# Performance work log

Measured on AMD Instinct MI355X. Metric: run time of the kernel, lower is better.

## Reference

```python
import jax, jax.numpy as jnp
import numpy as np

B, T, D, H = 256, 512, 64, 128


def setup_inputs() -> dict:
    key = jax.random.key(0)
    ks = jax.random.split(key, 24)
    inp = {
        'values': jax.random.normal(ks[0], (B, T, D), jnp.float32),
        'masks': jax.random.randint(ks[1], (B, T, D), 0, 2).astype(jnp.float32),
        'deltas': jax.random.uniform(ks[2], (B, T, D), jnp.float32),
        'empirical_mean': jax.random.normal(ks[3], (D,), jnp.float32),
        'X_filledLOCF': jax.random.normal(ks[4], (B, T, D), jnp.float32),
        # parameters (xavier-ish scale for matrices, uniform for vectors)
        'w_gamma_x': jax.random.uniform(ks[5], (D,), jnp.float32),
        'w_gamma_h': jax.random.normal(ks[6], (D, H), jnp.float32) * (2.0 / (D + H)) ** 0.5,
        'w_rx': jax.random.normal(ks[7], (D, H), jnp.float32) * (2.0 / (D + H)) ** 0.5,
        'w_rh': jax.random.normal(ks[8], (H, H), jnp.float32) * (1.0 / H) ** 0.5,
        'w_rm': jax.random.normal(ks[9], (D, H), jnp.float32) * (2.0 / (D + H)) ** 0.5,
        'w_zx': jax.random.normal(ks[10], (D, H), jnp.float32) * (2.0 / (D + H)) ** 0.5,
        'w_zh': jax.random.normal(ks[11], (H, H), jnp.float32) * (1.0 / H) ** 0.5,
        'w_zm': jax.random.normal(ks[12], (D, H), jnp.float32) * (2.0 / (D + H)) ** 0.5,
        'w_hx': jax.random.normal(ks[13], (D, H), jnp.float32) * (2.0 / (D + H)) ** 0.5,
        'w_hh': jax.random.normal(ks[14], (H, H), jnp.float32) * (1.0 / H) ** 0.5,
        'w_hm': jax.random.normal(ks[15], (D, H), jnp.float32) * (2.0 / (D + H)) ** 0.5,
        'b_gamma_x': jax.random.uniform(ks[16], (D,), jnp.float32),
        'b_gamma_h': jax.random.uniform(ks[17], (H,), jnp.float32),
        'b_r': jax.random.uniform(ks[18], (H,), jnp.float32),
        'b_z': jax.random.uniform(ks[19], (H,), jnp.float32),
        'b_h': jax.random.uniform(ks[20], (H,), jnp.float32),
    }
    return inp


def reference(values, masks, deltas, empirical_mean, X_filledLOCF,
              w_gamma_x, w_gamma_h, w_rx, w_rh, w_rm, w_zx, w_zh, w_zm,
              w_hx, w_hh, w_hm, b_gamma_x, b_gamma_h, b_r, b_z, b_h):
    b, t, d = values.shape
    h0 = jnp.zeros((b, w_gamma_h.shape[1]), values.dtype)

    def step(h, xs):
        x, m, dlt, xl = xs  # each [B, D]
        gamma_x = jnp.exp(-jax.nn.relu(w_gamma_x * dlt + b_gamma_x))      # [B, D]
        gamma_h = jnp.exp(-jax.nn.relu(dlt @ w_gamma_h + b_gamma_h))      # [B, H]
        x = m * x + (1 - m) * (gamma_x * xl + (1 - gamma_x) * empirical_mean)
        h = gamma_h * h
        z = jax.nn.sigmoid(x @ w_zx + h @ w_zh + m @ w_zm + b_z)
        r = jax.nn.sigmoid(x @ w_rx + h @ w_rh + m @ w_rm + b_r)
        h_tilde = jnp.tanh(x @ w_hx + (r * h) @ w_hh + m @ w_hm + b_h)
        h = (1 - z) * h + z * h_tilde
        return h, h

    # scan over time axis: [T, B, D]
    xs = (jnp.swapaxes(values, 0, 1), jnp.swapaxes(masks, 0, 1),
          jnp.swapaxes(deltas, 0, 1), jnp.swapaxes(X_filledLOCF, 0, 1))
    h_last, hs = jax.lax.scan(step, h0, xs)
    hidden_tensor = jnp.swapaxes(hs, 0, 1)  # [B, T, H]
    return hidden_tensor, h_last
```

## Files before the change

### kernel.cpp

```cpp
#include <hip/hip_runtime.h>
#include <hip/hip_fp16.h>

#define B_ 256
#define T_ 512
#define D_ 64
#define H_ 128
#define BB 16

typedef float f32x4 __attribute__((ext_vector_type(4)));
typedef short s16x4 __attribute__((ext_vector_type(4)));
typedef short s16x8 __attribute__((ext_vector_type(8)));
typedef __fp16 fp16x2 __attribute__((ext_vector_type(2)));
typedef _Float16 h16x4 __attribute__((ext_vector_type(4)));
typedef _Float16 f16x8v __attribute__((ext_vector_type(8)));

__device__ unsigned short g_W16[7 * 8 * 2 * 512];
__device__ float g_bias[512];

__device__ inline float fsig(float x) {
  return __builtin_amdgcn_rcpf(1.f + __expf(-x));
}
__device__ inline float ftanh(float x) {
  return 1.f - 2.f * __builtin_amdgcn_rcpf(1.f + __expf(2.f * x));
}
__device__ __forceinline__ f32x4 MFH(s16x8 a, s16x8 b, f32x4 c) {
  return __builtin_amdgcn_mfma_f32_16x16x32_f16(
      __builtin_bit_cast(f16x8v, a), __builtin_bit_cast(f16x8v, b), c, 0, 0, 0);
}
__device__ __forceinline__ f32x4 MFH2(s16x8 wfrag, f16x8v xfrag, f32x4 c) {
  return __builtin_amdgcn_mfma_f32_16x16x32_f16(
      __builtin_bit_cast(f16x8v, wfrag), xfrag, c, 0, 0, 0);
}

#define BAR()                                              \
  do {                                                     \
    asm volatile("s_waitcnt lgkmcnt(0)" ::: "memory");     \
    __builtin_amdgcn_s_barrier();                          \
  } while (0)

__global__ __launch_bounds__(64) void wprep(
    const float* __restrict__ wgh, const float* __restrict__ wzx,
    const float* __restrict__ wzm, const float* __restrict__ wrx,
    const float* __restrict__ wrm, const float* __restrict__ whx,
    const float* __restrict__ whm, const float* __restrict__ bgh,
    const float* __restrict__ bz, const float* __restrict__ br,
    const float* __restrict__ bh) {
  const int g = blockIdx.x, l = threadIdx.x;
  if (g < 112) {
    const float* mats[7] = {wgh, wzx, wzm, wrx, wrm, whx, whm};
    const int mat = g >> 4, sub = g & 15, ct = sub >> 1, tau = sub & 1;
    const float* W = mats[mat];
    const int base = ((mat * 8 + ct) * 2 + tau) * 512 + l * 8;
#pragma unroll
    for (int j = 0; j < 8; ++j) {
      const int k = 8 * (l >> 4) + j + 32 * tau;
      const int col = ct * 16 + (l & 15);
      g_W16[base + j] =
          __builtin_bit_cast(unsigned short, __float2half(W[k * 128 + col]));
    }
  } else {
    const int c = (g - 112) * 64 + l;
    float v = (c < 128)   ? bgh[c]
              : (c < 256) ? bz[c - 128]
              : (c < 384) ? br[c - 256]
                          : bh[c - 384];
    g_bias[c] = v;
  }
}

__global__ __launch_bounds__(256) void grud_pre_mfma(
    const float* __restrict__ values, const float* __restrict__ masks,
    const float* __restrict__ deltas, const float* __restrict__ emean,
    const float* __restrict__ locf, const float* __restrict__ w_gamma_x,
    const float* __restrict__ b_gamma_x, __half* __restrict__ A) {
  __shared__ __align__(16) char plds[25344];
  float* c_wg = (float*)(plds + 24576);
  float* c_bg = (float*)(plds + 24832);
  float* c_mn = (float*)(plds + 25088);

  const int tid = threadIdx.x;
  const int rowbase = blockIdx.x * 64;

  if (tid < 64) c_wg[tid] = w_gamma_x[tid];
  else if (tid < 128) c_bg[tid - 64] = b_gamma_x[tid - 64];
  else if (tid < 192) c_mn[tid - 128] = emean[tid - 128];
  __syncthreads();

  {
    const int r = tid >> 2;
    const int sp = tid & 3;
    const int swz = (r & 7) << 4;
#pragma unroll
    for (int ss = 0; ss < 2; ++ss) {
      const int s = sp + 4 * ss;
      const int k0 = 8 * s;
      const size_t gb = (size_t)(rowbase + r) * 64 + k0;
      const float4* vp = (const float4*)(values + gb);
      const float4* mp = (const float4*)(masks + gb);
      const float4* dp = (const float4*)(deltas + gb);
      const float4* lp = (const float4*)(locf + gb);
      float4 v0 = vp[0], v1 = vp[1], m0 = mp[0], m1 = mp[1];
      float4 d0 = dp[0], d1 = dp[1], l0 = lp[0], l1 = lp[1];
      float vv[8] = {v0.x, v0.y, v0.z, v0.w, v1.x, v1.y, v1.z, v1.w};
      float mm[8] = {m0.x, m0.y, m0.z, m0.w, m1.x, m1.y, m1.z, m1.w};
      float dd[8] = {d0.x, d0.y, d0.z, d0.w, d1.x, d1.y, d1.z, d1.w};
      float ll[8] = {l0.x, l0.y, l0.z, l0.w, l1.x, l1.y, l1.z, l1.w};
      s16x8 xe_, mv_, dl_;
#pragma unroll
      for (int j = 0; j < 8; ++j) {
        const int d_ = k0 + j;
        float gx = __expf(-fmaxf(c_wg[d_] * dd[j] + c_bg[d_], 0.f));
        float xo = mm[j] * vv[j] +
                   (1.f - mm[j]) * (gx * ll[j] + (1.f - gx) * c_mn[d_]);
        xe_[j] = __builtin_bit_cast(short, __float2half(xo));
        mv_[j] = __builtin_bit_cast(short, __float2half(mm[j]));
        dl_[j] = __builtin_bit_cast(short, __float2half(dd[j]));
      }
      const int ta = r * 128 + ((s * 16) ^ swz);
      *(s16x8*)(plds + ta) = xe_;
      *(s16x8*)(plds + 8192 + ta) = mv_;
      *(s16x8*)(plds + 16384 + ta) = dl_;
    }
  }
  __syncthreads();

  const int l = tid & 63;
  const int rt = tid >> 6;
  f16x8v xe0, xe1, mm0, mm1, dl0, dl1;
  {
    const int r = rt * 16 + (l & 15);
    const int swz = (r & 7) << 4;
    const int s0 = ((l >> 4) * 16) ^ swz;
    const int s1 = (((l >> 4) + 4) * 16) ^ swz;
    xe0 = *(const f16x8v*)(plds + r * 128 + s0);
    xe1 = *(const f16x8v*)(plds + r * 128 + s1);
    mm0 = *(const f16x8v*)(plds + 8192 + r * 128 + s0);
    mm1 = *(const f16x8v*)(plds + 8192 + r * 128 + s1);
    dl0 = *(const f16x8v*)(plds + 16384 + r * 128 + s0);
    dl1 = *(const f16x8v*)(plds + 16384 + r * 128 + s1);
  }

  const s16x8* Wb = (const s16x8*)g_W16;
  const int cj = (l >> 4) * 4;
  const int row = rowbase + rt * 16 + (l & 15);
  unsigned short* Aout = (unsigned short*)A + (size_t)row * 512;
#pragma unroll 4
  for (int ct = 0; ct < 32; ++ct) {
    const int g = ct >> 3, ctl = ct & 7;
    f32x4 acc = {0.f, 0.f, 0.f, 0.f};
    if (g == 0) {
      s16x8 B0 = Wb[(ctl * 2 + 0) * 64 + l];
      s16x8 B1 = Wb[(ctl * 2 + 1) * 64 + l];
      acc = MFH2(B0, dl0, acc);
      acc = MFH2(B1, dl1, acc);
    } else {
      const int mx = 2 * g - 1, mmat = 2 * g;
      s16x8 Bx0 = Wb[((mx * 8 + ctl) * 2 + 0) * 64 + l];
      s16x8 Bx1 = Wb[((mx * 8 + ctl) * 2 + 1) * 64 + l];
      s16x8 Bm0 = Wb[((mmat * 8 + ctl) * 2 + 0) * 64 + l];
      s16x8 Bm1 = Wb[((mmat * 8 + ctl) * 2 + 1) * 64 + l];
      acc = MFH2(Bx0, xe0, acc);
      acc = MFH2(Bx1, xe1, acc);
      acc = MFH2(Bm0, mm0, acc);
      acc = MFH2(Bm1, mm1, acc);
    }
    const f32x4 bv = *(const f32x4*)(g_bias + ct * 16 + cj);
    h16x4 outv;
#pragma unroll
    for (int j = 0; j < 4; ++j) {
      float v = acc[j] + bv[j];
      if (ct < 8) v = __expf(-fmaxf(v, 0.f));
      outv[j] = (_Float16)v;
    }
    *(h16x4*)(Aout + g * 128 + ctl * 16 + cj) = outv;
  }
}

#define STEP(T0, CUR, NXT)                                                  \
  do {                                                                      \
    const int t_ = (T0);                                                    \
    f32x4 Dz0 = {(float)CUR[1][0], (float)CUR[1][1],                        \
                 (float)CUR[1][2], (float)CUR[1][3]};                       \
    f32x4 Dr0 = {(float)CUR[2][0], (float)CUR[2][1],                        \
                 (float)CUR[2][2], (float)CUR[2][3]};                       \
    f32x4 Dh0 = {(float)CUR[3][0], (float)CUR[3][1],                        \
                 (float)CUR[3][2], (float)CUR[3][3]};                       \
    {                                         \
      const int t4 = (t_ + 4 < T_) ? t_ + 4 : T_ - 1;                       \
      const size_t r = ((size_t)bg * T_ + t4) * 128 + ci;                   \
      CUR[0] = Arows[r];       CUR[1] = Arows[r + 32];                      \
      CUR[2] = Arows[r + 64];  CUR[3] = Arows[r + 96];                      \
    }                                                                       \
    f32x4 Dz1 = {0, 0, 0, 0}, Dr1 = {0, 0, 0, 0};                           \
    {                                                                       \
      s16x8 bh0 = *(const s16x8*)(h_bf + off_rd[0]);                        \
      s16x8 bh1 = *(const s16x8*)(h_bf + off_rd[1]);                        \
      s16x8 bh2 = *(const s16x8*)(h_bf + off_rd[2]);                        \
      s16x8 bh3 = *(const s16x8*)(h_bf + off_rd[3]);                        \
      Dz0 = MFH(wzf[0], bh0, Dz0); Dr0 = MFH(wrf[0], bh0, Dr0);             \
      Dz1 = MFH(wzf[2], bh2, Dz1); Dr1 = MFH(wrf[2], bh2, Dr1);             \
      Dz0 = MFH(wzf[1], bh1, Dz0); Dr0 = MFH(wrf[1], bh1, Dr0);             \
      Dz1 = MFH(wzf[3], bh3, Dz1); Dr1 = MFH(wrf[3], bh3, Dr1);             \
    }                                                                       \
    f32x4 zz;                                                               \
    {                                                                       \
      float r0_ = fsig(Dr0[0] + Dr1[0]) * hsc[0];                           \
      float r1_ = fsig(Dr0[1] + Dr1[1]) * hsc[1];                           \
      float r2_ = fsig(Dr0[2] + Dr1[2]) * hsc[2];                           \
      float r3_ = fsig(Dr0[3] + Dr1[3]) * hsc[3];                           \
      zz[0] = fsig(Dz0[0] + Dz1[0]); zz[1] = fsig(Dz0[1] + Dz1[1]);         \
      zz[2] = fsig(Dz0[2] + Dz1[2]); zz[3] = fsig(Dz0[3] + Dz1[3]);         \
      union { fp16x2 h2[2]; s16x4 v; } u;                                   \
      u.h2[0] = __builtin_amdgcn_cvt_pkrtz(r0_, r1_);                       \
      u.h2[1] = __builtin_amdgcn_cvt_pkrtz(r2_, r3_);                       \
      *(s16x4*)(rh_bf + off_wr) = u.v;                                      \
    }                                                                       \
    BAR();                                                                  \
    f32x4 Dh1 = {0, 0, 0, 0};                                               \
    {                                                                       \
      s16x8 p0 = *(const s16x8*)(rh_bf + off_rd[0]);                        \
      s16x8 p1 = *(const s16x8*)(rh_bf + off_rd[1]);                        \
      s16x8 p2 = *(const s16x8*)(rh_bf + off_rd[2]);                        \
      s16x8 p3 = *(const s16x8*)(rh_bf + off_rd[3]);                        \
      Dh0 = MFH(whf[0], p0, Dh0); Dh1 = MFH(whf[2], p2, Dh1);               \
      Dh0 = MFH(whf[1], p1, Dh0); Dh1 = MFH(whf[3], p3, Dh1);               \
    }                                                                       \
    f32x4 hnv, hgv;                                                         \
    _Pragma("unroll")                                                       \
    for (int j = 0; j < 4; ++j) {                                           \
      float ht = ftanh(Dh0[j] + Dh1[j]);                                    \
      float hn = hsc[j] + zz[j] * (ht - hsc[j]);                            \
      hnv[j] = hn;                                                          \
      float hg = hn * (float)NXT[0][j];              \
      hgv[j] = hg;                                                          \
      hsc[j] = hg;                                                          \
    }                                                                       \
    {                                                                       \
      union { fp16x2 h2[2]; s16x4 v; } u;                                   \
      u.h2[0] = __builtin_amdgcn_cvt_pkrtz(hgv[0], hgv[1]);                 \
      u.h2[1] = __builtin_amdgcn_cvt_pkrtz(hgv[2], hgv[3]);                 \
      *(s16x4*)(h_bf + off_wr) = u.v;                                       \
    }                                                                       \
    *(f32x4*)(hid + ((size_t)bg * T_ + t_) * H_ + cb) = hnv;                \
    if (t_ == T_ - 1) *(f32x4*)(hlast + (size_t)bg * H_ + cb) = hnv;        \
    BAR();                                                                  \
  } while (0)

__global__ __launch_bounds__(512, 1) void grud_rec_mfma(
    const __half* __restrict__ A, const float* __restrict__ w_zh,
    const float* __restrict__ w_rh, const float* __restrict__ w_hh,
    float* __restrict__ hid, float* __restrict__ hlast) {
  const int tid = threadIdx.x;
  const int w = tid >> 6;
  const int lane = tid & 63;
  const int b = lane & 15;
  const int q = lane >> 4;
  const int cb = w * 16 + q * 4;
  const int bg = blockIdx.x * BB + b;

  __shared__ __align__(16) char lds[8192];
  char* h_bf = lds;
  char* rh_bf = lds + 4096;

  s16x8 wzf[4], wrf[4], whf[4];
#pragma unroll
  for (int tau = 0; tau < 4; ++tau) {
    s16x8 az, ar, ah;
#pragma unroll
    for (int j = 0; j < 8; ++j) {
      const int k = q * 8 + j + 32 * tau;
      az[j] = __builtin_bit_cast(short, (_Float16)w_zh[k * H_ + w * 16 + b]);
      ar[j] = __builtin_bit_cast(short, (_Float16)w_rh[k * H_ + w * 16 + b]);
      ah[j] = __builtin_bit_cast(short, (_Float16)w_hh[k * H_ + w * 16 + b]);
    }
    wzf[tau] = az; wrf[tau] = ar; whf[tau] = ah;
  }

  for (int i = tid; i < 8192 / 16; i += 512)
    ((f32x4*)lds)[i] = f32x4{0.f, 0.f, 0.f, 0.f};

  int off_rd[4];
#pragma unroll
  for (int tau = 0; tau < 4; ++tau) off_rd[tau] = tau * 1024 + lane * 16;
  const int off_wr =
      (w >> 1) * 1024 + (b + 16 * ((2 * w + (q >> 1)) & 3)) * 16 + 8 * (q & 1);

  const h16x4* Arows = (const h16x4*)A;
  const int ci = cb >> 2;

  h16x4 b0[4], b1[4], b2[4], b3[4];
  {
    const size_t r0 = ((size_t)bg * T_ + 0) * 128 + ci;
    b0[0] = Arows[r0]; b0[1] = Arows[r0 + 32];
    b0[2] = Arows[r0 + 64]; b0[3] = Arows[r0 + 96];
    const size_t r1 = ((size_t)bg * T_ + 1) * 128 + ci;
    b1[0] = Arows[r1]; b1[1] = Arows[r1 + 32];
    b1[2] = Arows[r1 + 64]; b1[3] = Arows[r1 + 96];
    const size_t r2 = ((size_t)bg * T_ + 2) * 128 + ci;
    b2[0] = Arows[r2]; b2[1] = Arows[r2 + 32];
    b2[2] = Arows[r2 + 64]; b2[3] = Arows[r2 + 96];
    const size_t r3 = ((size_t)bg * T_ + 3) * 128 + ci;
    b3[0] = Arows[r3]; b3[1] = Arows[r3 + 32];
    b3[2] = Arows[r3 + 64]; b3[3] = Arows[r3 + 96];
  }
  f32x4 hsc = {0.f, 0.f, 0.f, 0.f};
  __syncthreads();

  for (int tp = 0; tp < T_; tp += 4) {
    STEP(tp + 0, b0, b1);
    STEP(tp + 1, b1, b2);
    STEP(tp + 2, b2, b3);
    STEP(tp + 3, b3, b0);
  }
}

extern "C" void kernel_launch(void* const* d_in, const int* in_sizes, int n_in,
                              void* d_out, int out_size, void* d_ws, size_t ws_size,
                              hipStream_t stream) {
  const float* values = (const float*)d_in[0];
  const float* masks = (const float*)d_in[1];
  const float* deltas = (const float*)d_in[2];
  const float* emean = (const float*)d_in[3];
  const float* locf = (const float*)d_in[4];
  const float* w_gamma_x = (const float*)d_in[5];
  const float* w_gamma_h = (const float*)d_in[6];
  const float* w_rx = (const float*)d_in[7];
  const float* w_rh = (const float*)d_in[8];
  const float* w_rm = (const float*)d_in[9];
  const float* w_zx = (const float*)d_in[10];
  const float* w_zh = (const float*)d_in[11];
  const float* w_zm = (const float*)d_in[12];
  const float* w_hx = (const float*)d_in[13];
  const float* w_hh = (const float*)d_in[14];
  const float* w_hm = (const float*)d_in[15];
  const float* b_gamma_x = (const float*)d_in[16];
  const float* b_gamma_h = (const float*)d_in[17];
  const float* b_r = (const float*)d_in[18];
  const float* b_z = (const float*)d_in[19];
  const float* b_h = (const float*)d_in[20];

  float* hid = (float*)d_out;
  float* hlast = hid + (size_t)B_ * T_ * H_;
  __half* A = (__half*)d_ws;

  wprep<<<dim3(120), dim3(64), 0, stream>>>(
      w_gamma_h, w_zx, w_zm, w_rx, w_rm, w_hx, w_hm, b_gamma_h, b_z, b_r, b_h);
  grud_pre_mfma<<<dim3(B_ * T_ / 64), dim3(256), 0, stream>>>(
      values, masks, deltas, emean, locf, w_gamma_x, b_gamma_x, A);
  grud_rec_mfma<<<dim3(B_ / BB), dim3(512), 0, stream>>>(A, w_zh, w_rh, w_hh,
                                                         hid, hlast);
}
```

Before: 631.0 us.

## Process two 16-row batch groups per block to interleave independent recurrences

Each block now handles 32 batch rows as two independent 16-row groups (A and B), so their MFMA chains and activations interleave inside one step. The aim is to hide MFMA and LDS latency on the serial recurrence critical path with independent work, and to spread the per-step barrier cost over twice as many rows. In exchange the grid is halved to 8 blocks, so fewer CUs are used, and register pressure rises with the doubled prefetch buffers. The dual-accumulator split per gate is replaced by a single longer accumulation chain per group.

```diff
diff --git a/kernel.cpp b/kernel.cpp
--- a/kernel.cpp
+++ b/kernel.cpp
@@ -5,7 +5,7 @@
 #define T_ 512
 #define D_ 64
 #define H_ 128
-#define BB 16
+#define BB 32
 
 typedef float f32x4 __attribute__((ext_vector_type(4)));
 typedef short s16x4 __attribute__((ext_vector_type(4)));
@@ -179,70 +179,105 @@
 #define STEP(T0, CUR, NXT)                                                  \
   do {                                                                      \
     const int t_ = (T0);                                                    \
-    f32x4 Dz0 = {(float)CUR[1][0], (float)CUR[1][1],                        \
+    f32x4 DzA = {(float)CUR[1][0], (float)CUR[1][1],                        \
                  (float)CUR[1][2], (float)CUR[1][3]};                       \
-    f32x4 Dr0 = {(float)CUR[2][0], (float)CUR[2][1],                        \
+    f32x4 DrA = {(float)CUR[2][0], (float)CUR[2][1],                        \
                  (float)CUR[2][2], (float)CUR[2][3]};                       \
-    f32x4 Dh0 = {(float)CUR[3][0], (float)CUR[3][1],                        \
+    f32x4 DhA = {(float)CUR[3][0], (float)CUR[3][1],                        \
                  (float)CUR[3][2], (float)CUR[3][3]};                       \
-    {                                         \
+    f32x4 DzB = {(float)CUR[5][0], (float)CUR[5][1],                        \
+                 (float)CUR[5][2], (float)CUR[5][3]};                       \
+    f32x4 DrB = {(float)CUR[6][0], (float)CUR[6][1],                        \
+                 (float)CUR[6][2], (float)CUR[6][3]};                       \
+    f32x4 DhB = {(float)CUR[7][0], (float)CUR[7][1],                        \
+                 (float)CUR[7][2], (float)CUR[7][3]};                       \
+    {                            \
       const int t4 = (t_ + 4 < T_) ? t_ + 4 : T_ - 1;                       \
-      const size_t r = ((size_t)bg * T_ + t4) * 128 + ci;                   \
-      CUR[0] = Arows[r];       CUR[1] = Arows[r + 32];                      \
-      CUR[2] = Arows[r + 64];  CUR[3] = Arows[r + 96];                      \
-    }                                                                       \
-    f32x4 Dz1 = {0, 0, 0, 0}, Dr1 = {0, 0, 0, 0};                           \
+      const size_t rA = ((size_t)bgA * T_ + t4) * 128 + ci;                 \
+      const size_t rB = ((size_t)bgB * T_ + t4) * 128 + ci;                 \
+      CUR[0] = Arows[rA];       CUR[1] = Arows[rA + 32];                    \
+      CUR[2] = Arows[rA + 64];  CUR[3] = Arows[rA + 96];                    \
+      CUR[4] = Arows[rB];       CUR[5] = Arows[rB + 32];                    \
+      CUR[6] = Arows[rB + 64];  CUR[7] = Arows[rB + 96];                    \
+    }                                                                       \
     {                                                                       \
-      s16x8 bh0 = *(const s16x8*)(h_bf + off_rd[0]);                        \
-      s16x8 bh1 = *(const s16x8*)(h_bf + off_rd[1]);                        \
-      s16x8 bh2 = *(const s16x8*)(h_bf + off_rd[2]);                        \
-      s16x8 bh3 = *(const s16x8*)(h_bf + off_rd[3]);                        \
-      Dz0 = MFH(wzf[0], bh0, Dz0); Dr0 = MFH(wrf[0], bh0, Dr0);             \
-      Dz1 = MFH(wzf[2], bh2, Dz1); Dr1 = MFH(wrf[2], bh2, Dr1);             \
-      Dz0 = MFH(wzf[1], bh1, Dz0); Dr0 = MFH(wrf[1], bh1, Dr0);             \
-      Dz1 = MFH(wzf[3], bh3, Dz1); Dr1 = MFH(wrf[3], bh3, Dr1);             \
-    }                                                                       \
-    f32x4 zz;                                                               \
+      s16x8 hA0 = *(const s16x8*)(lds + off_rd[0]);                         \
+      s16x8 hA1 = *(const s16x8*)(lds + off_rd[1]);                         \
+      s16x8 hA2 = *(const s16x8*)(lds + off_rd[2]);                         \
+      s16x8 hA3 = *(const s16x8*)(lds + off_rd[3]);                         \
+      s16x8 hB0 = *(const s16x8*)(lds + 8192 + off_rd[0]);                  \
+      s16x8 hB1 = *(const s16x8*)(lds + 8192 + off_rd[1]);                  \
+      s16x8 hB2 = *(const s16x8*)(lds + 8192 + off_rd[2]);                  \
+      s16x8 hB3 = *(const s16x8*)(lds + 8192 + off_rd[3]);                  \
+      DzA = MFH(wzf[0], hA0, DzA); DzB = MFH(wzf[0], hB0, DzB);             \
+      DrA = MFH(wrf[0], hA0, DrA); DrB = MFH(wrf[0], hB0, DrB);             \
+      DzA = MFH(wzf[1], hA1, DzA); DzB = MFH(wzf[1], hB1, DzB);             \
+      DrA = MFH(wrf[1], hA1, DrA); DrB = MFH(wrf[1], hB1, DrB);             \
+      DzA = MFH(wzf[2], hA2, DzA); DzB = MFH(wzf[2], hB2, DzB);             \
+      DrA = MFH(wrf[2], hA2, DrA); DrB = MFH(wrf[2], hB2, DrB);             \
+      DzA = MFH(wzf[3], hA3, DzA); DzB = MFH(wzf[3], hB3, DzB);             \
+      DrA = MFH(wrf[3], hA3, DrA); DrB = MFH(wrf[3], hB3, DrB);             \
+    }                                                                       \
+    f32x4 zzA, zzB;                                                         \
     {                                                                       \
-      float r0_ = fsig(Dr0[0] + Dr1[0]) * hsc[0];                           \
-      float r1_ = fsig(Dr0[1] + Dr1[1]) * hsc[1];                           \
-      float r2_ = fsig(Dr0[2] + Dr1[2]) * hsc[2];                           \
-      float r3_ = fsig(Dr0[3] + Dr1[3]) * hsc[3];                           \
-      zz[0] = fsig(Dz0[0] + Dz1[0]); zz[1] = fsig(Dz0[1] + Dz1[1]);         \
-      zz[2] = fsig(Dz0[2] + Dz1[2]); zz[3] = fsig(Dz0[3] + Dz1[3]);         \
-      union { fp16x2 h2[2]; s16x4 v; } u;                                   \
-      u.h2[0] = __builtin_amdgcn_cvt_pkrtz(r0_, r1_);                       \
-      u.h2[1] = __builtin_amdgcn_cvt_pkrtz(r2_, r3_);                       \
-      *(s16x4*)(rh_bf + off_wr) = u.v;                                      \
+      union { fp16x2 h2[2]; s16x4 v; } uA, uB;                              \
+      float a0 = fsig(DrA[0]) * hscA[0], a1 = fsig(DrA[1]) * hscA[1];       \
+      float a2 = fsig(DrA[2]) * hscA[2], a3 = fsig(DrA[3]) * hscA[3];       \
+      float b0_ = fsig(DrB[0]) * hscB[0], b1_ = fsig(DrB[1]) * hscB[1];     \
+      float b2_ = fsig(DrB[2]) * hscB[2], b3_ = fsig(DrB[3]) * hscB[3];     \
+      zzA[0] = fsig(DzA[0]); zzA[1] = fsig(DzA[1]);                         \
+      zzA[2] = fsig(DzA[2]); zzA[3] = fsig(DzA[3]);                         \
+      zzB[0] = fsig(DzB[0]); zzB[1] = fsig(DzB[1]);                         \
+      zzB[2] = fsig(DzB[2]); zzB[3] = fsig(DzB[3]);                         \
+      uA.h2[0] = __builtin_amdgcn_cvt_pkrtz(a0, a1);                        \
+      uA.h2[1] = __builtin_amdgcn_cvt_pkrtz(a2, a3);                        \
+      uB.h2[0] = __builtin_amdgcn_cvt_pkrtz(b0_, b1_);                      \
+      uB.h2[1] = __builtin_amdgcn_cvt_pkrtz(b2_, b3_);                      \
+      *(s16x4*)(lds + 4096 + off_wr) = uA.v;                                \
+      *(s16x4*)(lds + 12288 + off_wr) = uB.v;                               \
     }                                                                       \
     BAR();                                                                  \
-    f32x4 Dh1 = {0, 0, 0, 0};                                               \
     {                                                                       \
-      s16x8 p0 = *(const s16x8*)(rh_bf + off_rd[0]);                        \
-      s16x8 p1 = *(const s16x8*)(rh_bf + off_rd[1]);                        \
-      s16x8 p2 = *(const s16x8*)(rh_bf + off_rd[2]);                        \
-      s16x8 p3 = *(const s16x8*)(rh_bf + off_rd[3]);                        \
-      Dh0 = MFH(whf[0], p0, Dh0); Dh1 = MFH(whf[2], p2, Dh1);               \
-      Dh0 = MFH(whf[1], p1, Dh0); Dh1 = MFH(whf[3], p3, Dh1);               \
-    }                                                                       \
-    f32x4 hnv, hgv;                                                         \
-    _Pragma("unroll")                                                       \
-    for (int j = 0; j < 4; ++j) {                                           \
-      float ht = ftanh(Dh0[j] + Dh1[j]);                                    \
-      float hn = hsc[j] + zz[j] * (ht - hsc[j]);                            \
-      hnv[j] = hn;                                                          \
-      float hg = hn * (float)NXT[0][j];              \
-      hgv[j] = hg;                                                          \
-      hsc[j] = hg;                                                          \
+      s16x8 pA0 = *(const s16x8*)(lds + 4096 + off_rd[0]);                  \
+      s16x8 pA1 = *(const s16x8*)(lds + 4096 + off_rd[1]);                  \
+      s16x8 pA2 = *(const s16x8*)(lds + 4096 + off_rd[2]);                  \
+      s16x8 pA3 = *(const s16x8*)(lds + 4096 + off_rd[3]);                  \
+      s16x8 pB0 = *(const s16x8*)(lds + 12288 + off_rd[0]);                 \
+      s16x8 pB1 = *(const s16x8*)(lds + 12288 + off_rd[1]);                 \
+      s16x8 pB2 = *(const s16x8*)(lds + 12288 + off_rd[2]);                 \
+      s16x8 pB3 = *(const s16x8*)(lds + 12288 + off_rd[3]);                 \
+      DhA = MFH(whf[0], pA0, DhA); DhB = MFH(whf[0], pB0, DhB);             \
+      DhA = MFH(whf[1], pA1, DhA); DhB = MFH(whf[1], pB1, DhB);             \
+      DhA = MFH(whf[2], pA2, DhA); DhB = MFH(whf[2], pB2, DhB);             \
+      DhA = MFH(whf[3], pA3, DhA); DhB = MFH(whf[3], pB3, DhB);             \
     }                                                                       \
     {                                                                       \
-      union { fp16x2 h2[2]; s16x4 v; } u;                                   \
-      u.h2[0] = __builtin_amdgcn_cvt_pkrtz(hgv[0], hgv[1]);                 \
-      u.h2[1] = __builtin_amdgcn_cvt_pkrtz(hgv[2], hgv[3]);                 \
-      *(s16x4*)(h_bf + off_wr) = u.v;                                       \
-    }                                                                       \
-    *(f32x4*)(hid + ((size_t)bg * T_ + t_) * H_ + cb) = hnv;                \
-    if (t_ == T_ - 1) *(f32x4*)(hlast + (size_t)bg * H_ + cb) = hnv;        \
+      f32x4 hnA, hnB;                                                       \
+      union { fp16x2 h2[2]; s16x4 v; } uA, uB;                              \
+      _Pragma("unroll")                                                     \
+      for (int j = 0; j < 4; ++j) {                                         \
+        float htA = ftanh(DhA[j]);                                          \
+        float ha = hscA[j] + zzA[j] * (htA - hscA[j]);                      \
+        hnA[j] = ha;                                                        \
+        hscA[j] = ha * (float)NXT[0][j];                                    \
+        float htB = ftanh(DhB[j]);                                          \
+        float hb = hscB[j] + zzB[j] * (htB - hscB[j]);                      \
+        hnB[j] = hb;                                                        \
+        hscB[j] = hb * (float)NXT[4][j];                                    \
+      }                                                                     \
+      uA.h2[0] = __builtin_amdgcn_cvt_pkrtz(hscA[0], hscA[1]);              \
+      uA.h2[1] = __builtin_amdgcn_cvt_pkrtz(hscA[2], hscA[3]);              \
+      uB.h2[0] = __builtin_amdgcn_cvt_pkrtz(hscB[0], hscB[1]);              \
+      uB.h2[1] = __builtin_amdgcn_cvt_pkrtz(hscB[2], hscB[3]);              \
+      *(s16x4*)(lds + off_wr) = uA.v;                                       \
+      *(s16x4*)(lds + 8192 + off_wr) = uB.v;                                \
+      *(f32x4*)(hid + ((size_t)bgA * T_ + t_) * H_ + cb) = hnA;             \
+      *(f32x4*)(hid + ((size_t)bgB * T_ + t_) * H_ + cb) = hnB;             \
+      if (t_ == T_ - 1) {                                                   \
+        *(f32x4*)(hlast + (size_t)bgA * H_ + cb) = hnA;                     \
+        *(f32x4*)(hlast + (size_t)bgB * H_ + cb) = hnB;                     \
+      }                                                                     \
+    }                                                                       \
     BAR();                                                                  \
   } while (0)
 
@@ -256,11 +291,10 @@
   const int b = lane & 15;
   const int q = lane >> 4;
   const int cb = w * 16 + q * 4;
-  const int bg = blockIdx.x * BB + b;
-
-  __shared__ __align__(16) char lds[8192];
-  char* h_bf = lds;
-  char* rh_bf = lds + 4096;
+  const int bgA = blockIdx.x * BB + b;
+  const int bgB = bgA + 16;
+
+  __shared__ __align__(16) char lds[16384];
 
   s16x8 wzf[4], wrf[4], whf[4];
 #pragma unroll
@@ -276,7 +310,7 @@
     wzf[tau] = az; wrf[tau] = ar; whf[tau] = ah;
   }
 
-  for (int i = tid; i < 8192 / 16; i += 512)
+  for (int i = tid; i < 16384 / 16; i += 512)
     ((f32x4*)lds)[i] = f32x4{0.f, 0.f, 0.f, 0.f};
 
   int off_rd[4];
@@ -288,22 +322,18 @@
   const h16x4* Arows = (const h16x4*)A;
   const int ci = cb >> 2;
 
-  h16x4 b0[4], b1[4], b2[4], b3[4];
-  {
-    const size_t r0 = ((size_t)bg * T_ + 0) * 128 + ci;
-    b0[0] = Arows[r0]; b0[1] = Arows[r0 + 32];
-    b0[2] = Arows[r0 + 64]; b0[3] = Arows[r0 + 96];
-    const size_t r1 = ((size_t)bg * T_ + 1) * 128 + ci;
-    b1[0] = Arows[r1]; b1[1] = Arows[r1 + 32];
-    b1[2] = Arows[r1 + 64]; b1[3] = Arows[r1 + 96];
-    const size_t r2 = ((size_t)bg * T_ + 2) * 128 + ci;
-    b2[0] = Arows[r2]; b2[1] = Arows[r2 + 32];
-    b2[2] = Arows[r2 + 64]; b2[3] = Arows[r2 + 96];
-    const size_t r3 = ((size_t)bg * T_ + 3) * 128 + ci;
-    b3[0] = Arows[r3]; b3[1] = Arows[r3 + 32];
-    b3[2] = Arows[r3 + 64]; b3[3] = Arows[r3 + 96];
-  }
-  f32x4 hsc = {0.f, 0.f, 0.f, 0.f};
+  h16x4 b0[8], b1[8], b2[8], b3[8];
+#pragma unroll
+  for (int t0 = 0; t0 < 4; ++t0) {
+    h16x4* dst = (t0 == 0) ? b0 : (t0 == 1) ? b1 : (t0 == 2) ? b2 : b3;
+    const size_t rA = ((size_t)bgA * T_ + t0) * 128 + ci;
+    const size_t rB = ((size_t)bgB * T_ + t0) * 128 + ci;
+    dst[0] = Arows[rA];       dst[1] = Arows[rA + 32];
+    dst[2] = Arows[rA + 64];  dst[3] = Arows[rA + 96];
+    dst[4] = Arows[rB];       dst[5] = Arows[rB + 32];
+    dst[6] = Arows[rB + 64];  dst[7] = Arows[rB + 96];
+  }
+  f32x4 hscA = {0.f, 0.f, 0.f, 0.f}, hscB = {0.f, 0.f, 0.f, 0.f};
   __syncthreads();
 
   for (int tp = 0; tp < T_; tp += 4) {
```

Result: slower. 1.192 ms (+88.8%).
